# Kernel optimization log

Hardware: AMD Instinct MI355X
Metric: run time of the kernel (lower is better)

Reference implementation:

```python
import jax, jax.numpy as jnp
import numpy as np

B, S, H, V, L = 8, 1024, 1024, 512, 6
NEG_INF = -10000000.0  # matches torch neg_inf constant


def setup_inputs() -> dict:
    key = jax.random.key(0)
    ks = jax.random.split(key, 13)
    s = 0.02
    return {
        "inputs": jax.random.randint(ks[0], (B, S), 0, V),
        "embedding": jax.random.normal(ks[1], (V, H), jnp.float32) * s,
        "Wq": jax.random.normal(ks[2], (L, H, H), jnp.float32) * s,
        "bq": jnp.zeros((L, H), jnp.float32),
        "Wk": jax.random.normal(ks[3], (L, H, H), jnp.float32) * s,
        "bk": jnp.zeros((L, H), jnp.float32),
        "Wv": jax.random.normal(ks[4], (L, H, H), jnp.float32) * s,
        "bv": jnp.zeros((L, H), jnp.float32),
        "Wm": jax.random.normal(ks[5], (L, H, H), jnp.float32) * s,
        "bm": jnp.zeros((L, H), jnp.float32),
        "Wout": jax.random.normal(ks[6], (H, V), jnp.float32) * s,
        "bout": jnp.zeros((V,), jnp.float32),
    }


def reference(inputs, embedding, Wq, bq, Wk, bk, Wv, bv, Wm, bm, Wout, bout):
    Hd = embedding.shape[1]
    seq = inputs.shape[1]
    scale = jax.lax.rsqrt(jnp.asarray(Hd, jnp.float32))
    idx = jnp.arange(seq)
    # mask[key, query]: additive NEG_INF where key > query (strict lower triangle)
    mask = jnp.where(idx[:, None] > idx[None, :], jnp.float32(NEG_INF), jnp.float32(0.0))
    x = embedding[inputs]  # [B, S, H]
    n_layers = Wq.shape[0]
    attns = []
    for l in range(n_layers):
        q = x @ Wq[l] + bq[l]
        k = x @ Wk[l] + bk[l]
        v = x @ Wv[l] + bv[l]
        # [B, key, query], softmax over key axis (dim=1), exactly as original
        logits = jnp.einsum('bkh,bqh->bkq', k, q) * scale + mask
        attn = jax.nn.softmax(logits, axis=1)
        ctx = jnp.einsum('bkq,bkh->bqh', attn, v)  # attn^T @ v
        residual = x + ctx
        x = residual + jax.nn.relu(ctx @ Wm[l] + bm[l])
        attns.append(attn)
    out = x @ Wout + bout  # [B, S, V]
    return out, jnp.stack(attns)  # attns: [L, B, S, S]
```

## Files before the change

### kernel.cpp

```cpp
#include <hip/hip_runtime.h>
#include <stdint.h>

typedef unsigned short u16;
typedef unsigned int u32;
typedef __bf16 bf16x8 __attribute__((ext_vector_type(8)));
typedef float floatx4 __attribute__((ext_vector_type(4)));

#define NEG_INF_F (-10000000.0f)

__device__ __forceinline__ float bf2f(u16 u) {
    union { u32 u; float f; } x; x.u = ((u32)u) << 16; return x.f;
}
__device__ __forceinline__ u16 f2bf(float f) {
    union { float f; u32 u; } x; x.f = f;
    u32 r = x.u + 0x7fffu + ((x.u >> 16) & 1u);
    return (u16)(r >> 16);
}

__device__ __forceinline__ void async_cp16(const void* g, void* l) {
    __builtin_amdgcn_global_load_lds(
        (const __attribute__((address_space(1))) void*)g,
        (__attribute__((address_space(3))) void*)l, 16, 0, 0);
}

enum { EPI_QKV = 0, EPI_LOGITS = 1, EPI_CTX = 2, EPI_MLP = 3, EPI_OUT = 4 };

template <int EPI>
__global__ __launch_bounds__(256) void gemm_bt(
    const u16* __restrict__ A, int lda, long long aBatch,
    const u16* __restrict__ B, int ldb, long long bBatch,
    void* __restrict__ Cv, int ldc, long long cBatch,
    int K,
    const float* __restrict__ bias,
    float* __restrict__ xbuf,
    const u16* __restrict__ ctxb,
    u16* __restrict__ xb,
    float scale)
{
    __shared__ __align__(16) u16 sA[128 * 64];
    __shared__ __align__(16) u16 sB[128 * 64];

    const int tid  = threadIdx.x;
    const int wave = tid >> 6;
    const int lane = tid & 63;
    const int bz   = blockIdx.z;

    int bxE = blockIdx.x, byE = blockIdx.y;
    if constexpr (EPI == EPI_LOGITS) {
        const int t = blockIdx.x;
        int tq = (int)((sqrtf(8.0f * t + 1.0f) - 1.0f) * 0.5f);
        while ((tq + 1) * (tq + 2) / 2 <= t) ++tq;
        while (tq * (tq + 1) / 2 > t) --tq;
        bxE = tq;
        byE = t - tq * (tq + 1) / 2;
    }
    int Keff = K;
    if constexpr (EPI == EPI_CTX) Keff = min(K, (byE + 1) * 128);

    const u16* Ab = A + (long long)bz * aBatch + (long long)(byE * 128) * lda;
    const u16* Bb = B + (long long)bz * bBatch + (long long)(bxE * 128) * ldb;

    const int wm = wave >> 1, wn = wave & 1;
    const int quad = lane >> 4;

    const int srowoff = lane >> 3;
    const int gf      = (lane & 7) ^ ((lane >> 3) & 7);

    const int ra = 64 * wm + (lane & 15);
    const int rb = 64 * wn + (lane & 15);
    const int rx7 = lane & 7;

    floatx4 zero = {0.f, 0.f, 0.f, 0.f};
    floatx4 acc[4][4];
#pragma unroll
    for (int i = 0; i < 4; ++i)
#pragma unroll
        for (int j = 0; j < 4; ++j) acc[i][j] = zero;

    for (int k0 = 0; k0 < Keff; k0 += 64) {
#pragma unroll
        for (int i = 0; i < 4; ++i) {
            const int c = wave * 4 + i;
            const int r = c * 8 + srowoff;
            async_cp16(Ab + (long long)r * lda + k0 + gf * 8, &sA[c * 512 + lane * 8]);
            async_cp16(Bb + (long long)r * ldb + k0 + gf * 8, &sB[c * 512 + lane * 8]);
        }
        __syncthreads();

#pragma unroll
        for (int kk = 0; kk < 64; kk += 32) {
            const int gbase = kk >> 3;
            const int ga = ((gbase + quad) ^ rx7) << 3;
            bf16x8 af[4], bf[4];
#pragma unroll
            for (int mi = 0; mi < 4; ++mi)
                af[mi] = *(const bf16x8*)&sA[(ra + 16 * mi) * 64 + ga];
#pragma unroll
            for (int ni = 0; ni < 4; ++ni)
                bf[ni] = *(const bf16x8*)&sB[(rb + 16 * ni) * 64 + ga];
#pragma unroll
            for (int mi = 0; mi < 4; ++mi)
#pragma unroll
                for (int ni = 0; ni < 4; ++ni)
                    acc[mi][ni] = __builtin_amdgcn_mfma_f32_16x16x32_bf16(
                        af[mi], bf[ni], acc[mi][ni], 0, 0, 0);
        }
        __syncthreads();
    }

    const int m0 = byE * 128 + 64 * wm + (quad << 2);
    const int n0 = bxE * 128 + 64 * wn + (lane & 15);
#pragma unroll
    for (int mi = 0; mi < 4; ++mi) {
#pragma unroll
        for (int ni = 0; ni < 4; ++ni) {
            const int gn = n0 + ni * 16;
#pragma unroll
            for (int r = 0; r < 4; ++r) {
                const int gm = m0 + mi * 16 + r;
                float v = acc[mi][ni][r];
                if constexpr (EPI == EPI_QKV) {
                    v += bias[gn];
                    ((u16*)Cv)[(long long)bz * cBatch + (long long)gm * ldc + gn] = f2bf(v);
                } else if constexpr (EPI == EPI_LOGITS) {
                    v = v * scale + (gm > gn ? NEG_INF_F : 0.0f);
                    ((float*)Cv)[(long long)bz * cBatch + (long long)gm * ldc + gn] = v;
                } else if constexpr (EPI == EPI_CTX) {
                    ((u16*)Cv)[(long long)bz * cBatch + (long long)gm * ldc + gn] = f2bf(v);
                } else if constexpr (EPI == EPI_MLP) {
                    const long long idx = (long long)gm * ldc + gn;
                    v += bias[gn];
                    v = fmaxf(v, 0.0f);
                    float xv = xbuf[idx] + bf2f(ctxb[idx]) + v;
                    xbuf[idx] = xv;
                    xb[idx]   = f2bf(xv);
                } else {
                    v += bias[gn];
                    ((float*)Cv)[(long long)gm * ldc + gn] = v;
                }
            }
        }
    }
}

template <typename Tin>
__global__ void transpose_bf16(const Tin* __restrict__ in, int inStride, long long inBatch,
                               u16* __restrict__ out, int outStride, long long outBatch)
{
    __shared__ float tile[64][65];
    const Tin* ib = in + (long long)blockIdx.z * inBatch;
    u16* ob       = out + (long long)blockIdx.z * outBatch;
    const int r0 = blockIdx.y * 64, c0 = blockIdx.x * 64;
    const int x = threadIdx.x, y = threadIdx.y;
#pragma unroll
    for (int j = 0; j < 16; ++j) {
        int r = y + j * 4;
        float v;
        if constexpr (sizeof(Tin) == 2)
            v = bf2f(((const u16*)ib)[(long long)(r0 + r) * inStride + c0 + x]);
        else
            v = ((const float*)ib)[(long long)(r0 + r) * inStride + c0 + x];
        tile[r][x] = v;
    }
    __syncthreads();
#pragma unroll
    for (int j = 0; j < 16; ++j) {
        int r = y + j * 4;
        ob[(long long)(c0 + r) * outStride + r0 + x] = f2bf(tile[x][r]);
    }
}

template <int L, int H, int V>
__global__ void setup_weights(const float* __restrict__ Wq, const float* __restrict__ Wk,
                              const float* __restrict__ Wv, const float* __restrict__ Wm,
                              const float* __restrict__ Wout,
                              const float* __restrict__ bq, const float* __restrict__ bk,
                              const float* __restrict__ bv,
                              u16* __restrict__ WqkvT, u16* __restrict__ WmT,
                              u16* __restrict__ WoutT, float* __restrict__ bqkv)
{
    const int z = blockIdx.z;
    if (z == 4 * L + 1) {
        int i = ((blockIdx.y * 16 + blockIdx.x) * 256) + threadIdx.y * 64 + threadIdx.x;
        if (i < L * 3 * H) {
            int l = i / (3 * H), j = i % (3 * H);
            float v = (j < H) ? bq[l * H + j]
                    : (j < 2 * H) ? bk[l * H + j - H]
                                  : bv[l * H + j - 2 * H];
            bqkv[i] = v;
        }
        return;
    }

    const float* in;
    u16* outp;
    int inStride, outStride;
    if (z == 4 * L) {
        if (blockIdx.x >= V / 64) return;
        in = Wout; inStride = V;
        outp = WoutT; outStride = H;
    } else {
        const int which = z / L, l = z % L;
        inStride = H; outStride = H;
        if (which == 3) { in = Wm + (long long)l * H * H; outp = WmT + (long long)l * H * H; }
        else {
            in   = (which == 0 ? Wq : which == 1 ? Wk : Wv) + (long long)l * H * H;
            outp = WqkvT + (long long)l * 3 * H * H + (long long)which * H * H;
        }
    }

    __shared__ float tile[64][65];
    const int r0 = blockIdx.y * 64, c0 = blockIdx.x * 64;
    const int x = threadIdx.x, y = threadIdx.y;
#pragma unroll
    for (int j = 0; j < 16; ++j) {
        int r = y + j * 4;
        tile[r][x] = in[(long long)(r0 + r) * inStride + c0 + x];
    }
    __syncthreads();
#pragma unroll
    for (int j = 0; j < 16; ++j) {
        int r = y + j * 4;
        outp[(long long)(c0 + r) * outStride + r0 + x] = f2bf(tile[x][r]);
    }
}

__global__ __launch_bounds__(1024) void softmax_emit(
    float* __restrict__ attn, long long batchStride,
    u16* __restrict__ attnT, long long tBatchStride)
{
    __shared__ float sm[64][16], sl[64][16], sm2[8][16], sl2[8][16];
    __shared__ float sM[16], sInv[16];

    float* base = attn + (long long)blockIdx.y * batchStride;
    const int x = threadIdx.x, ky = threadIdx.y;
    const int q = blockIdx.x * 16 + x;

    float v[16];
    float m = -3.4e38f, l = 0.f;
#pragma unroll
    for (int j = 0; j < 16; ++j) {
        const int k = ky * 16 + j;
        float vj = NEG_INF_F;
        if (k <= q) vj = base[(long long)k * 1024 + q];
        v[j] = vj;
        float mn = fmaxf(m, vj);
        l = l * __expf(m - mn) + __expf(vj - mn);
        m = mn;
    }
    sm[ky][x] = m;
    sl[ky][x] = l;
    __syncthreads();
    if (ky < 8) {
        float M = -3.4e38f, L = 0.f;
#pragma unroll
        for (int t = 0; t < 8; ++t) {
            float mm = sm[ky + 8 * t][x], ll = sl[ky + 8 * t][x];
            float mn = fmaxf(M, mm);
            L = L * __expf(M - mn) + ll * __expf(mm - mn);
            M = mn;
        }
        sm2[ky][x] = M;
        sl2[ky][x] = L;
    }
    __syncthreads();
    if (ky == 0) {
        float M = -3.4e38f, L = 0.f;
#pragma unroll
        for (int t = 0; t < 8; ++t) {
            float mm = sm2[t][x], ll = sl2[t][x];
            float mn = fmaxf(M, mm);
            L = L * __expf(M - mn) + ll * __expf(mm - mn);
            M = mn;
        }
        sM[x]   = M;
        sInv[x] = 1.0f / L;
    }
    __syncthreads();
    const float M = sM[x], inv = sInv[x];

    u16 pb[16];
#pragma unroll
    for (int j = 0; j < 16; ++j) {
        float p = __expf(v[j] - M) * inv;
        base[(long long)(ky * 16 + j) * 1024 + q] = p;
        pb[j] = f2bf(p);
    }
    u16* trow = attnT + (long long)blockIdx.y * tBatchStride + (long long)q * 1024 + ky * 16;
    ((uint4*)trow)[0] = *(const uint4*)&pb[0];
    ((uint4*)trow)[1] = *(const uint4*)&pb[8];
}

__global__ void embed_kernel(const int* __restrict__ tok, const float* __restrict__ emb,
                             float* __restrict__ x, u16* __restrict__ xb)
{
    const int row = blockIdx.x;
    const int t   = tok[row];
    float4 v = ((const float4*)(emb + (long long)t * 1024))[threadIdx.x];
    ((float4*)(x + (long long)row * 1024))[threadIdx.x] = v;
    uint2 p;
    p.x = (u32)f2bf(v.x) | ((u32)f2bf(v.y) << 16);
    p.y = (u32)f2bf(v.z) | ((u32)f2bf(v.w) << 16);
    ((uint2*)(xb + (long long)row * 1024))[threadIdx.x] = p;
}

extern "C" void kernel_launch(void* const* d_in, const int* in_sizes, int n_in,
                              void* d_out, int out_size, void* d_ws, size_t ws_size,
                              hipStream_t stream)
{
    const int*   tok  = (const int*)d_in[0];
    const float* emb  = (const float*)d_in[1];
    const float* Wq   = (const float*)d_in[2];
    const float* bq   = (const float*)d_in[3];
    const float* Wk   = (const float*)d_in[4];
    const float* bk   = (const float*)d_in[5];
    const float* Wv   = (const float*)d_in[6];
    const float* bv   = (const float*)d_in[7];
    const float* Wm   = (const float*)d_in[8];
    const float* bm   = (const float*)d_in[9];
    const float* Wout = (const float*)d_in[10];
    const float* bout = (const float*)d_in[11];
    float* out = (float*)d_out;

    constexpr int B = 8, S = 1024, H = 1024, V = 512, L = 6;
    constexpr long long M = (long long)B * S;

    char* ws = (char*)d_ws;
    u16*   WqkvT = (u16*)ws;   ws += (long long)L * 3 * H * H * 2;
    u16*   WmT   = (u16*)ws;   ws += (long long)L * H * H * 2;
    u16*   WoutT = (u16*)ws;   ws += (long long)V * H * 2;
    float* bqkv  = (float*)ws; ws += (long long)L * 3 * H * 4;
    float* x     = (float*)ws; ws += M * H * 4;
    u16*   xb    = (u16*)ws;   ws += M * H * 2;
    u16*   QKV   = (u16*)ws;   ws += M * 3 * H * 2;
    u16*   attnT = (u16*)ws;   ws += (long long)B * S * S * 2;
    u16*   Vt    = (u16*)ws;   ws += (long long)B * S * S * 2;
    u16*   ctxb  = (u16*)ws;   ws += M * H * 2;

    float* attnOut = out + (long long)B * S * V;

    setup_weights<L, H, V><<<dim3(16, 16, 4 * L + 2), dim3(64, 4), 0, stream>>>(
        Wq, Wk, Wv, Wm, Wout, bq, bk, bv, WqkvT, WmT, WoutT, bqkv);
    embed_kernel<<<M, 256, 0, stream>>>(tok, emb, x, xb);

    for (int l = 0; l < L; ++l) {
        gemm_bt<EPI_QKV><<<dim3(3 * H / 128, M / 128, 1), 256, 0, stream>>>(
            xb, H, 0, WqkvT + (long long)l * 3 * H * H, H, 0,
            QKV, 3 * H, 0, H, bqkv + l * 3 * H, nullptr, nullptr, nullptr, 0.f);

        float* attnL = attnOut + (long long)l * B * S * S;
        gemm_bt<EPI_LOGITS><<<dim3(36, 1, B), 256, 0, stream>>>(
            QKV + H, 3 * H, (long long)S * 3 * H,
            QKV, 3 * H, (long long)S * 3 * H,
            attnL, S, (long long)S * S, H,
            nullptr, nullptr, nullptr, nullptr, 0.03125f);

        softmax_emit<<<dim3(S / 16, B), dim3(16, 64), 0, stream>>>(
            attnL, (long long)S * S, attnT, (long long)S * S);

        transpose_bf16<u16><<<dim3(16, 16, B), dim3(64, 4), 0, stream>>>(
            QKV + 2 * H, 3 * H, (long long)S * 3 * H, Vt, S, (long long)S * S);

        gemm_bt<EPI_CTX><<<dim3(H / 128, S / 128, B), 256, 0, stream>>>(
            attnT, S, (long long)S * S, Vt, S, (long long)S * S,
            ctxb, H, (long long)S * H, S,
            nullptr, nullptr, nullptr, nullptr, 0.f);

        gemm_bt<EPI_MLP><<<dim3(H / 128, M / 128, 1), 256, 0, stream>>>(
            ctxb, H, 0, WmT + (long long)l * H * H, H, 0,
            nullptr, H, 0, H, bm + l * H, x, ctxb, xb, 0.f);
    }

    gemm_bt<EPI_OUT><<<dim3(V / 128, M / 128, 1), 256, 0, stream>>>(
        xb, H, 0, WoutT, H, 0, out, V, 0, H,
        bout, nullptr, nullptr, nullptr, 0.f);
}
```

Baseline: 1.490 ms.

## Remap GEMM grids for XCD locality, merge V-transpose into softmax, drop fp32 residual

Flattens every GEMM grid to 1D and remaps block indices so that blocks sharing operands (same batch or same tile column) land on the same XCD (blockIdx&7), which targets L2 reuse on the chiplet layout. The separate V transpose kernel is folded into the softmax kernel as extra grid zones, saving one launch per layer. The fp32 residual stream x is removed and the residual is kept only in bf16, which cuts memory traffic in the MLP epilogue but adds rounding error that accumulates across layers.

```diff
diff --git a/kernel.cpp b/kernel.cpp
--- a/kernel.cpp
+++ b/kernel.cpp
@@ -32,10 +32,9 @@
     void* __restrict__ Cv, int ldc, long long cBatch,
     int K,
     const float* __restrict__ bias,
-    float* __restrict__ xbuf,
     const u16* __restrict__ ctxb,
     u16* __restrict__ xb,
-    float scale)
+    float scale, int nx, int ny)
 {
     __shared__ __align__(16) u16 sA[128 * 64];
     __shared__ __align__(16) u16 sB[128 * 64];
@@ -43,16 +42,26 @@
     const int tid  = threadIdx.x;
     const int wave = tid >> 6;
     const int lane = tid & 63;
-    const int bz   = blockIdx.z;
-
-    int bxE = blockIdx.x, byE = blockIdx.y;
+
+    int bxE, byE, bz;
     if constexpr (EPI == EPI_LOGITS) {
-        const int t = blockIdx.x;
+        bz = blockIdx.x & 7;
+        int t = blockIdx.x >> 3;
         int tq = (int)((sqrtf(8.0f * t + 1.0f) - 1.0f) * 0.5f);
         while ((tq + 1) * (tq + 2) / 2 <= t) ++tq;
         while (tq * (tq + 1) / 2 > t) --tq;
         bxE = tq;
         byE = t - tq * (tq + 1) / 2;
+    } else if constexpr (EPI == EPI_CTX) {
+        bz = blockIdx.x & 7;
+        int t = blockIdx.x >> 3;
+        bxE = t & 7;
+        byE = t >> 3;
+    } else {
+        bz = 0;
+        const int k = blockIdx.x & 7, r = blockIdx.x >> 3;
+        if (nx >= 8) { const int xp = nx >> 3; bxE = xp * k + (r % xp); byE = r / xp; }
+        else         { bxE = k >> 1; byE = (k & 1) * (ny >> 1) + r; }
     }
     int Keff = K;
     if constexpr (EPI == EPI_CTX) Keff = min(K, (byE + 1) * 128);
@@ -121,7 +130,7 @@
                 float v = acc[mi][ni][r];
                 if constexpr (EPI == EPI_QKV) {
                     v += bias[gn];
-                    ((u16*)Cv)[(long long)bz * cBatch + (long long)gm * ldc + gn] = f2bf(v);
+                    ((u16*)Cv)[(long long)gm * ldc + gn] = f2bf(v);
                 } else if constexpr (EPI == EPI_LOGITS) {
                     v = v * scale + (gm > gn ? NEG_INF_F : 0.0f);
                     ((float*)Cv)[(long long)bz * cBatch + (long long)gm * ldc + gn] = v;
@@ -131,42 +140,14 @@
                     const long long idx = (long long)gm * ldc + gn;
                     v += bias[gn];
                     v = fmaxf(v, 0.0f);
-                    float xv = xbuf[idx] + bf2f(ctxb[idx]) + v;
-                    xbuf[idx] = xv;
-                    xb[idx]   = f2bf(xv);
+                    float xv = bf2f(xb[idx]) + bf2f(ctxb[idx]) + v;
+                    xb[idx] = f2bf(xv);
                 } else {
                     v += bias[gn];
                     ((float*)Cv)[(long long)gm * ldc + gn] = v;
                 }
             }
         }
-    }
-}
-
-template <typename Tin>
-__global__ void transpose_bf16(const Tin* __restrict__ in, int inStride, long long inBatch,
-                               u16* __restrict__ out, int outStride, long long outBatch)
-{
-    __shared__ float tile[64][65];
-    const Tin* ib = in + (long long)blockIdx.z * inBatch;
-    u16* ob       = out + (long long)blockIdx.z * outBatch;
-    const int r0 = blockIdx.y * 64, c0 = blockIdx.x * 64;
-    const int x = threadIdx.x, y = threadIdx.y;
-#pragma unroll
-    for (int j = 0; j < 16; ++j) {
-        int r = y + j * 4;
-        float v;
-        if constexpr (sizeof(Tin) == 2)
-            v = bf2f(((const u16*)ib)[(long long)(r0 + r) * inStride + c0 + x]);
-        else
-            v = ((const float*)ib)[(long long)(r0 + r) * inStride + c0 + x];
-        tile[r][x] = v;
-    }
-    __syncthreads();
-#pragma unroll
-    for (int j = 0; j < 16; ++j) {
-        int r = y + j * 4;
-        ob[(long long)(c0 + r) * outStride + r0 + x] = f2bf(tile[x][r]);
     }
 }
 
@@ -225,79 +206,106 @@
     }
 }
 
-__global__ __launch_bounds__(1024) void softmax_emit(
-    float* __restrict__ attn, long long batchStride,
-    u16* __restrict__ attnT, long long tBatchStride)
-{
-    __shared__ float sm[64][16], sl[64][16], sm2[8][16], sl2[8][16];
-    __shared__ float sM[16], sInv[16];
-
-    float* base = attn + (long long)blockIdx.y * batchStride;
-    const int x = threadIdx.x, ky = threadIdx.y;
-    const int q = blockIdx.x * 16 + x;
-
-    float v[16];
-    float m = -3.4e38f, l = 0.f;
-#pragma unroll
-    for (int j = 0; j < 16; ++j) {
-        const int k = ky * 16 + j;
-        float vj = NEG_INF_F;
-        if (k <= q) vj = base[(long long)k * 1024 + q];
-        v[j] = vj;
-        float mn = fmaxf(m, vj);
-        l = l * __expf(m - mn) + __expf(vj - mn);
-        m = mn;
-    }
-    sm[ky][x] = m;
-    sl[ky][x] = l;
-    __syncthreads();
-    if (ky < 8) {
-        float M = -3.4e38f, L = 0.f;
-#pragma unroll
-        for (int t = 0; t < 8; ++t) {
-            float mm = sm[ky + 8 * t][x], ll = sl[ky + 8 * t][x];
-            float mn = fmaxf(M, mm);
-            L = L * __expf(M - mn) + ll * __expf(mm - mn);
-            M = mn;
-        }
-        sm2[ky][x] = M;
-        sl2[ky][x] = L;
-    }
-    __syncthreads();
-    if (ky == 0) {
-        float M = -3.4e38f, L = 0.f;
-#pragma unroll
-        for (int t = 0; t < 8; ++t) {
-            float mm = sm2[t][x], ll = sl2[t][x];
-            float mn = fmaxf(M, mm);
-            L = L * __expf(M - mn) + ll * __expf(mm - mn);
-            M = mn;
-        }
-        sM[x]   = M;
-        sInv[x] = 1.0f / L;
-    }
-    __syncthreads();
-    const float M = sM[x], inv = sInv[x];
-
-    u16 pb[16];
-#pragma unroll
-    for (int j = 0; j < 16; ++j) {
-        float p = __expf(v[j] - M) * inv;
-        base[(long long)(ky * 16 + j) * 1024 + q] = p;
-        pb[j] = f2bf(p);
-    }
-    u16* trow = attnT + (long long)blockIdx.y * tBatchStride + (long long)q * 1024 + ky * 16;
-    ((uint4*)trow)[0] = *(const uint4*)&pb[0];
-    ((uint4*)trow)[1] = *(const uint4*)&pb[8];
+__global__ __launch_bounds__(1024) void attn_post(
+    float* __restrict__ attn, long long aStride,
+    u16* __restrict__ attnT, long long tStride,
+    const u16* __restrict__ qkv, u16* __restrict__ Vt)
+{
+    const int zone = blockIdx.y;
+    if (zone < 8) {
+        __shared__ float sm[64][16], sl[64][16], sm2[8][16], sl2[8][16];
+        __shared__ float sM[16], sInv[16];
+
+        float* base = attn + (long long)zone * aStride;
+        const int x = threadIdx.x, ky = threadIdx.y;
+        const int q = blockIdx.x * 16 + x;
+
+        float v[16];
+        float m = -3.4e38f, l = 0.f;
+#pragma unroll
+        for (int j = 0; j < 16; ++j) {
+            const int k = ky * 16 + j;
+            float vj = NEG_INF_F;
+            if (k <= q) vj = base[(long long)k * 1024 + q];
+            v[j] = vj;
+            float mn = fmaxf(m, vj);
+            l = l * __expf(m - mn) + __expf(vj - mn);
+            m = mn;
+        }
+        sm[ky][x] = m;
+        sl[ky][x] = l;
+        __syncthreads();
+        if (ky < 8) {
+            float M = -3.4e38f, L = 0.f;
+#pragma unroll
+            for (int t = 0; t < 8; ++t) {
+                float mm = sm[ky + 8 * t][x], ll = sl[ky + 8 * t][x];
+                float mn = fmaxf(M, mm);
+                L = L * __expf(M - mn) + ll * __expf(mm - mn);
+                M = mn;
+            }
+            sm2[ky][x] = M;
+            sl2[ky][x] = L;
+        }
+        __syncthreads();
+        if (ky == 0) {
+            float M = -3.4e38f, L = 0.f;
+#pragma unroll
+            for (int t = 0; t < 8; ++t) {
+                float mm = sm2[t][x], ll = sl2[t][x];
+                float mn = fmaxf(M, mm);
+                L = L * __expf(M - mn) + ll * __expf(mm - mn);
+                M = mn;
+            }
+            sM[x]   = M;
+            sInv[x] = 1.0f / L;
+        }
+        __syncthreads();
+        const float M = sM[x], inv = sInv[x];
+
+        u16 pb[16];
+#pragma unroll
+        for (int j = 0; j < 16; ++j) {
+            float p = __expf(v[j] - M) * inv;
+            base[(long long)(ky * 16 + j) * 1024 + q] = p;
+            pb[j] = f2bf(p);
+        }
+        u16* trow = attnT + (long long)zone * tStride + (long long)q * 1024 + ky * 16;
+        ((uint4*)trow)[0] = *(const uint4*)&pb[0];
+        ((uint4*)trow)[1] = *(const uint4*)&pb[8];
+    } else {
+        const int b = zone - 8;
+        const u16* Vb = qkv + 2 * 1024 + (long long)b * (1024LL * 3072);
+        u16* Ob       = Vt + (long long)b * (1024LL * 1024);
+        __shared__ float tile[64][65];
+        const int tid = threadIdx.y * 16 + threadIdx.x;
+        const int tx = tid & 63, ty = tid >> 6;
+#pragma unroll
+        for (int rep = 0; rep < 4; ++rep) {
+            const int T = blockIdx.x + rep * 64;
+            const int s0 = (T >> 4) * 64, h0 = (T & 15) * 64;
+            __syncthreads();
+#pragma unroll
+            for (int j = 0; j < 4; ++j) {
+                const int s = j * 16 + ty;
+                tile[s][tx] = bf2f(Vb[(long long)(s0 + s) * 3072 + h0 + tx]);
+            }
+            __syncthreads();
+#pragma unroll
+            for (int j = 0; j < 4; ++j) {
+                const int h = j * 16 + ty;
+                Ob[(long long)(h0 + h) * 1024 + s0 + tx] = f2bf(tile[tx][h]);
+            }
+        }
+    }
 }
 
 __global__ void embed_kernel(const int* __restrict__ tok, const float* __restrict__ emb,
-                             float* __restrict__ x, u16* __restrict__ xb)
+                             u16* __restrict__ xb)
 {
     const int row = blockIdx.x;
     const int t   = tok[row];
     float4 v = ((const float4*)(emb + (long long)t * 1024))[threadIdx.x];
-    ((float4*)(x + (long long)row * 1024))[threadIdx.x] = v;
     uint2 p;
     p.x = (u32)f2bf(v.x) | ((u32)f2bf(v.y) << 16);
     p.y = (u32)f2bf(v.z) | ((u32)f2bf(v.w) << 16);
@@ -330,7 +338,6 @@
     u16*   WmT   = (u16*)ws;   ws += (long long)L * H * H * 2;
     u16*   WoutT = (u16*)ws;   ws += (long long)V * H * 2;
     float* bqkv  = (float*)ws; ws += (long long)L * 3 * H * 4;
-    float* x     = (float*)ws; ws += M * H * 4;
     u16*   xb    = (u16*)ws;   ws += M * H * 2;
     u16*   QKV   = (u16*)ws;   ws += M * 3 * H * 2;
     u16*   attnT = (u16*)ws;   ws += (long long)B * S * S * 2;
@@ -341,37 +348,34 @@
 
     setup_weights<L, H, V><<<dim3(16, 16, 4 * L + 2), dim3(64, 4), 0, stream>>>(
         Wq, Wk, Wv, Wm, Wout, bq, bk, bv, WqkvT, WmT, WoutT, bqkv);
-    embed_kernel<<<M, 256, 0, stream>>>(tok, emb, x, xb);
+    embed_kernel<<<M, 256, 0, stream>>>(tok, emb, xb);
 
     for (int l = 0; l < L; ++l) {
-        gemm_bt<EPI_QKV><<<dim3(3 * H / 128, M / 128, 1), 256, 0, stream>>>(
+        gemm_bt<EPI_QKV><<<1536, 256, 0, stream>>>(
             xb, H, 0, WqkvT + (long long)l * 3 * H * H, H, 0,
-            QKV, 3 * H, 0, H, bqkv + l * 3 * H, nullptr, nullptr, nullptr, 0.f);
+            QKV, 3 * H, 0, H, bqkv + l * 3 * H, nullptr, nullptr, 0.f, 24, 64);
 
         float* attnL = attnOut + (long long)l * B * S * S;
-        gemm_bt<EPI_LOGITS><<<dim3(36, 1, B), 256, 0, stream>>>(
+        gemm_bt<EPI_LOGITS><<<288, 256, 0, stream>>>(
             QKV + H, 3 * H, (long long)S * 3 * H,
             QKV, 3 * H, (long long)S * 3 * H,
             attnL, S, (long long)S * S, H,
-            nullptr, nullptr, nullptr, nullptr, 0.03125f);
-
-        softmax_emit<<<dim3(S / 16, B), dim3(16, 64), 0, stream>>>(
-            attnL, (long long)S * S, attnT, (long long)S * S);
-
-        transpose_bf16<u16><<<dim3(16, 16, B), dim3(64, 4), 0, stream>>>(
-            QKV + 2 * H, 3 * H, (long long)S * 3 * H, Vt, S, (long long)S * S);
-
-        gemm_bt<EPI_CTX><<<dim3(H / 128, S / 128, B), 256, 0, stream>>>(
+            nullptr, nullptr, nullptr, 0.03125f, 0, 0);
+
+        attn_post<<<dim3(64, 16), dim3(16, 64), 0, stream>>>(
+            attnL, (long long)S * S, attnT, (long long)S * S, QKV, Vt);
+
+        gemm_bt<EPI_CTX><<<512, 256, 0, stream>>>(
             attnT, S, (long long)S * S, Vt, S, (long long)S * S,
             ctxb, H, (long long)S * H, S,
-            nullptr, nullptr, nullptr, nullptr, 0.f);
-
-        gemm_bt<EPI_MLP><<<dim3(H / 128, M / 128, 1), 256, 0, stream>>>(
+            nullptr, nullptr, nullptr, 0.f, 0, 0);
+
+        gemm_bt<EPI_MLP><<<512, 256, 0, stream>>>(
             ctxb, H, 0, WmT + (long long)l * H * H, H, 0,
-            nullptr, H, 0, H, bm + l * H, x, ctxb, xb, 0.f);
-    }
-
-    gemm_bt<EPI_OUT><<<dim3(V / 128, M / 128, 1), 256, 0, stream>>>(
+            nullptr, H, 0, H, bm + l * H, ctxb, xb, 0.f, 8, 64);
+    }
+
+    gemm_bt<EPI_OUT><<<256, 256, 0, stream>>>(
         xb, H, 0, WoutT, H, 0, out, V, 0, H,
-        bout, nullptr, nullptr, nullptr, 0.f);
-}
+        bout, nullptr, nullptr, 0.f, 4, 64);
+}
```

Result: faster. 1.355 ms (-9.0%).
